# Kernel optimization log

Hardware: AMD Instinct MI355X
Metric: run time of the kernel (lower is better)

Reference implementation:

```python
import jax, jax.numpy as jnp
import numpy as np
import math

B, N, D_IN, D_OUT, H = 8, 1024, 512, 512, 8
DH = D_OUT // H  # 64
SCALE = math.sqrt(DH)

def setup_inputs() -> dict:
    key = jax.random.key(0)
    ks = jax.random.split(key, 10)
    s_in = 1.0 / math.sqrt(D_IN)
    s_out = 1.0 / math.sqrt(D_OUT)
    return {
        "x": jax.random.normal(ks[0], (B, N, D_IN), dtype=jnp.float32),
        "Wq": jax.random.uniform(ks[1], (D_IN, D_OUT), jnp.float32, -s_in, s_in),
        "bq": jnp.zeros((D_OUT,), jnp.float32),
        "Wk": jax.random.uniform(ks[2], (D_IN, D_OUT), jnp.float32, -s_in, s_in),
        "bk": jnp.zeros((D_OUT,), jnp.float32),
        "Wv": jax.random.uniform(ks[3], (D_IN, D_OUT), jnp.float32, -s_in, s_in),
        "bv": jnp.zeros((D_OUT,), jnp.float32),
        "Wo": jax.random.uniform(ks[4], (D_OUT, D_OUT), jnp.float32, -s_out, s_out),
        "bo": jnp.zeros((D_OUT,), jnp.float32),
        # external distance-based positional bias buffer (num_heads, N, N)
        "pos_bias": 0.01 * jax.random.normal(ks[5], (H, N, N), dtype=jnp.float32),
    }

def reference(x, Wq, bq, Wk, bk, Wv, bv, Wo, bo, pos_bias):
    Bx, Nx, _ = x.shape
    # QKV projections -> (B, H, N, DH)
    def split_heads(t):
        return t.reshape(Bx, Nx, H, DH).transpose(0, 2, 1, 3)
    q = split_heads(x @ Wq + bq)
    k = split_heads(x @ Wk + bk)
    v = split_heads(x @ Wv + bv)
    # scaled dot-product scores with additive positional bias
    scores = jnp.einsum('bhnd,bhmd->bhnm', q, k) / SCALE + pos_bias[None]
    attn = jax.nn.softmax(scores, axis=-1)  # dropout p=0 (eval)
    out = jnp.einsum('bhnm,bhmd->bhnd', attn, v)
    out = out.transpose(0, 2, 1, 3).reshape(Bx, Nx, D_OUT)  # concat heads
    return out @ Wo + bo
```

## Files before the change

### kernel.cpp

```cpp
#include <hip/hip_runtime.h>
#include <hip/hip_bf16.h>
#include <stdint.h>


typedef __attribute__((ext_vector_type(4))) float f32x4;
typedef __attribute__((ext_vector_type(8))) short s16x8;
typedef __attribute__((ext_vector_type(4))) unsigned short u16x4;

union FragAB { s16x8 v; u16x4 h[2]; unsigned u[4]; };

#define LOG2E 1.44269504089f
#define QSCALE (0.125f * LOG2E)

__device__ __forceinline__ unsigned short f2b(float f) {
  unsigned u = __builtin_bit_cast(unsigned, f);
  u = (u + 0x7FFFu + ((u >> 16) & 1u)) >> 16;
  return (unsigned short)u;
}
__device__ __forceinline__ unsigned pack2(float lo, float hi) {
  return ((unsigned)f2b(hi) << 16) | (unsigned)f2b(lo);
}

__global__ __launch_bounds__(256) void prep_k(const float* __restrict__ x,
                                              unsigned short* __restrict__ xb,
                                              const float* __restrict__ W0,
                                              const float* __restrict__ W1,
                                              const float* __restrict__ W2,
                                              const float* __restrict__ W3,
                                              unsigned short* __restrict__ Wt) {
  __shared__ float ld[64][68];
  const int t = threadIdx.x;
  if (blockIdx.x < 4096) {
    int idx = blockIdx.x * 256 + t;
    f32x4 v = ((const f32x4*)x)[idx];
    u16x4 o;
#pragma unroll
    for (int j = 0; j < 4; j++) o[j] = f2b(v[j]);
    ((u16x4*)xb)[idx] = o;
    return;
  }
  const int bid2 = blockIdx.x - 4096;
  const int widx = bid2 >> 6;
  const int tile = bid2 & 63;
  const int trow = tile >> 3, tcol = tile & 7;
  const float* W = widx == 0 ? W0 : widx == 1 ? W1 : widx == 2 ? W2 : W3;
  const int r = t >> 2, cc = (t & 3) * 16;
  const float* src = W + (size_t)(trow * 64 + r) * 512 + tcol * 64 + cc;
#pragma unroll
  for (int u = 0; u < 4; u++)
    ((f32x4*)&ld[r][cc])[u] = ((const f32x4*)src)[u];
  __syncthreads();
  unsigned short* dst = Wt + ((size_t)widx << 18) + (size_t)(tcol * 64 + r) * 512 +
                        trow * 64 + cc;
#pragma unroll
  for (int u = 0; u < 4; u++) {
    u16x4 o;
#pragma unroll
    for (int e = 0; e < 4; e++) o[e] = f2b(ld[cc + u * 4 + e][r]);
    ((u16x4*)dst)[u] = o;
  }
}

__global__ __launch_bounds__(256, 2) void gemm_qkv_k(const unsigned short* __restrict__ A,
                                                     const unsigned short* __restrict__ Bt,
                                                     const float* __restrict__ bq,
                                                     const float* __restrict__ bk,
                                                     const float* __restrict__ bv,
                                                     unsigned short* __restrict__ outp) {
  __shared__ unsigned short At[2][128][36];
  __shared__ unsigned short Bts[2][128][36];
  const int tid = threadIdx.x;
  const int lane = tid & 63;
  const int w = tid >> 6;
  const int wm = w >> 1, wn = w & 1;
  const int g = lane >> 4, c = lane & 15;
  const int bn0 = (blockIdx.x % 12) * 128;
  const int bm0 = (blockIdx.x / 12) * 128;
  const int srow = tid >> 1;
  const int scol = (tid & 1) * 16;

  f32x4 acc[4][4];
#pragma unroll
  for (int i = 0; i < 4; i++)
#pragma unroll
    for (int j = 0; j < 4; j++) acc[i][j] = f32x4{0.f, 0.f, 0.f, 0.f};

  u16x4 ra[4], rb[4];
  auto ld = [&](int kt) {
    const u16x4* pa = (const u16x4*)(A + (size_t)(bm0 + srow) * 512 + kt * 32 + scol);
    const u16x4* pb = (const u16x4*)(Bt + (size_t)(bn0 + srow) * 512 + kt * 32 + scol);
#pragma unroll
    for (int j = 0; j < 4; j++) { ra[j] = pa[j]; rb[j] = pb[j]; }
  };
  auto st = [&](int b) {
    u16x4* da = (u16x4*)&At[b][srow][scol];
    u16x4* db = (u16x4*)&Bts[b][srow][scol];
#pragma unroll
    for (int j = 0; j < 4; j++) { da[j] = ra[j]; db[j] = rb[j]; }
  };

  ld(0); st(0);
  __syncthreads();

  for (int kt = 0; kt < 16; ++kt) {
    const int cb = kt & 1;
    if (kt < 15) ld(kt + 1);

    FragAB af[4], bf[4];
#pragma unroll
    for (int mi = 0; mi < 4; mi++) {
      const u16x4* p = (const u16x4*)&At[cb][wm * 64 + mi * 16 + c][g * 8];
      af[mi].h[0] = p[0]; af[mi].h[1] = p[1];
    }
#pragma unroll
    for (int ni = 0; ni < 4; ni++) {
      const u16x4* p = (const u16x4*)&Bts[cb][wn * 64 + ni * 16 + c][g * 8];
      bf[ni].h[0] = p[0]; bf[ni].h[1] = p[1];
    }
    __builtin_amdgcn_s_setprio(1);
#pragma unroll
    for (int mi = 0; mi < 4; mi++)
#pragma unroll
      for (int ni = 0; ni < 4; ni++)
        acc[mi][ni] = __builtin_amdgcn_mfma_f32_16x16x32_bf16(af[mi].v, bf[ni].v,
                                                              acc[mi][ni], 0, 0, 0);
    __builtin_amdgcn_s_setprio(0);

    if (kt < 15) {
      st(cb ^ 1);
      __syncthreads();
    }
  }

  const int qkv = (bn0 + wn * 64) >> 9;
  const float* bp = qkv == 0 ? bq : (qkv == 1 ? bk : bv);
  const float scale = qkv == 0 ? QSCALE : 1.0f;
#pragma unroll
  for (int mi = 0; mi < 4; mi++) {
#pragma unroll
    for (int ni = 0; ni < 4; ni++) {
      const int col = bn0 + wn * 64 + ni * 16 + c;
      const int c9 = col & 511;
      const float bvv = bp[c9];
#pragma unroll
      for (int m = 0; m < 4; m++) {
        const int row = bm0 + wm * 64 + mi * 16 + g * 4 + m;
        const float v = (acc[mi][ni][m] + bvv) * scale;
        const int b = row >> 10, n = row & 1023;
        const int hh = c9 >> 6, d = col & 63;
        outp[((size_t)qkv << 22) + ((size_t)((b << 3) + hh) << 16) +
             ((size_t)n << 6) + d] = f2b(v);
      }
    }
  }
}

__global__ __launch_bounds__(256, 2) void gemm_o_k(const unsigned short* __restrict__ A,
                                                   const unsigned short* __restrict__ Bt,
                                                   const float* __restrict__ bias,
                                                   float* __restrict__ outp) {
  __shared__ unsigned short At[2][128][36];
  __shared__ unsigned short Bts[2][128][36];
  const int tid = threadIdx.x;
  const int lane = tid & 63;
  const int w = tid >> 6;
  const int wm = w >> 1, wn = w & 1;
  const int g = lane >> 4, c = lane & 15;
  const int bn0 = (blockIdx.x & 3) * 128;
  const int bm0 = (blockIdx.x >> 2) * 128;
  const int srow = tid >> 1;
  const int scol = (tid & 1) * 16;

  f32x4 acc[4][4];
#pragma unroll
  for (int i = 0; i < 4; i++)
#pragma unroll
    for (int j = 0; j < 4; j++) acc[i][j] = f32x4{0.f, 0.f, 0.f, 0.f};

  u16x4 ra[4], rb[4];
  auto ld = [&](int kt) {
    const u16x4* pa = (const u16x4*)(A + (size_t)(bm0 + srow) * 512 + kt * 32 + scol);
    const u16x4* pb = (const u16x4*)(Bt + (size_t)(bn0 + srow) * 512 + kt * 32 + scol);
#pragma unroll
    for (int j = 0; j < 4; j++) { ra[j] = pa[j]; rb[j] = pb[j]; }
  };
  auto st = [&](int b) {
    u16x4* da = (u16x4*)&At[b][srow][scol];
    u16x4* db = (u16x4*)&Bts[b][srow][scol];
#pragma unroll
    for (int j = 0; j < 4; j++) { da[j] = ra[j]; db[j] = rb[j]; }
  };

  ld(0); st(0);
  __syncthreads();

  for (int kt = 0; kt < 16; ++kt) {
    const int cb = kt & 1;
    if (kt < 15) ld(kt + 1);

    FragAB af[4], bf[4];
#pragma unroll
    for (int mi = 0; mi < 4; mi++) {
      const u16x4* p = (const u16x4*)&At[cb][wm * 64 + mi * 16 + c][g * 8];
      af[mi].h[0] = p[0]; af[mi].h[1] = p[1];
    }
#pragma unroll
    for (int ni = 0; ni < 4; ni++) {
      const u16x4* p = (const u16x4*)&Bts[cb][wn * 64 + ni * 16 + c][g * 8];
      bf[ni].h[0] = p[0]; bf[ni].h[1] = p[1];
    }
    __builtin_amdgcn_s_setprio(1);
#pragma unroll
    for (int mi = 0; mi < 4; mi++)
#pragma unroll
      for (int ni = 0; ni < 4; ni++)
        acc[mi][ni] = __builtin_amdgcn_mfma_f32_16x16x32_bf16(af[mi].v, bf[ni].v,
                                                              acc[mi][ni], 0, 0, 0);
    __builtin_amdgcn_s_setprio(0);

    if (kt < 15) {
      st(cb ^ 1);
      __syncthreads();
    }
  }

#pragma unroll
  for (int mi = 0; mi < 4; mi++) {
#pragma unroll
    for (int ni = 0; ni < 4; ni++) {
      const int col = bn0 + wn * 64 + ni * 16 + c;
      const float bv = bias[col];
#pragma unroll
      for (int m = 0; m < 4; m++) {
        const int row = bm0 + wm * 64 + mi * 16 + g * 4 + m;
        outp[(size_t)row * 512 + col] = acc[mi][ni][m] + bv;
      }
    }
  }
}

__global__ __launch_bounds__(512, 4) void attn_k(const unsigned short* __restrict__ Qb,
                                                 const unsigned short* __restrict__ Kb,
                                                 const unsigned short* __restrict__ Vb,
                                                 const float* __restrict__ pos_bias,
                                                 unsigned short* __restrict__ ao) {
  __shared__ unsigned short Klds[2][64][68];
  __shared__ unsigned short Vtlds[2][64][68];
  __shared__ unsigned short Plds[8][16][68];

  const int tid = threadIdx.x;
  const int lane = tid & 63;
  const int w = tid >> 6;
  const int g = lane >> 4, c = lane & 15;
  const int L = blockIdx.x;
  const int qt = L >> 6;
  const int bh = (L & 7) + 8 * ((L >> 3) & 7);
  const int h = bh & 7;
  const size_t bhq = (size_t)bh << 16;
  const int q0 = qt * 128 + w * 16;

  FragAB aq[2];
#pragma unroll
  for (int kk = 0; kk < 2; kk++) {
    const u16x4* p =
        (const u16x4*)(Qb + bhq + ((size_t)(q0 + c) << 6) + kk * 32 + g * 8);
    aq[kk].h[0] = p[0]; aq[kk].h[1] = p[1];
  }

  f32x4 acco[4];
#pragma unroll
  for (int nd = 0; nd < 4; nd++) acco[nd] = f32x4{0.f, 0.f, 0.f, 0.f};
  float lsum = 0.f;

  const int krow = tid >> 4;
  const int kslot = (tid & 15) * 4;
  const int vd = tid & 63;
  const int vs = w;

  u16x4 kr[2], vr[2];
  auto stageLoad = [&](int k0n) {
    kr[0] = *(const u16x4*)(Kb + bhq + ((size_t)(k0n + krow) << 6) + kslot);
    kr[1] = *(const u16x4*)(Kb + bhq + ((size_t)(k0n + krow + 32) << 6) + kslot);
    const unsigned short* pv = Vb + bhq + ((size_t)(k0n + vs * 8) << 6) + vd;
    union { unsigned short s[8]; u16x4 v[2]; } vv;
#pragma unroll
    for (int j = 0; j < 8; j++) vv.s[j] = pv[(size_t)j << 6];
    vr[0] = vv.v[0]; vr[1] = vv.v[1];
  };
  auto stageWrite = [&](int b) {
    *(u16x4*)&Klds[b][krow][kslot] = kr[0];
    *(u16x4*)&Klds[b][krow + 32][kslot] = kr[1];
    *(u16x4*)&Vtlds[b][vd][vs * 8] = vr[0];
    *(u16x4*)&Vtlds[b][vd][vs * 8 + 4] = vr[1];
  };

  const float* pbB = pos_bias + ((size_t)h << 20) + ((size_t)(q0 + c) << 10) + 4 * g;

  stageLoad(0);
  stageWrite(0);
  __syncthreads();

  for (int kt = 0; kt < 16; ++kt) {
    const int buf = kt & 1;
    const int k0 = kt << 6;
    if (kt < 15) stageLoad(k0 + 64);

    f32x4 pb[4];
#pragma unroll
    for (int ni = 0; ni < 4; ni++) pb[ni] = *(const f32x4*)(pbB + k0 + 16 * ni);

    FragAB bk[4][2];
#pragma unroll
    for (int ni = 0; ni < 4; ni++)
#pragma unroll
      for (int kk = 0; kk < 2; kk++) {
        const u16x4* p = (const u16x4*)&Klds[buf][ni * 16 + c][kk * 32 + g * 8];
        bk[ni][kk].h[0] = p[0]; bk[ni][kk].h[1] = p[1];
      }
    f32x4 sT[4];
    __builtin_amdgcn_s_setprio(1);
#pragma unroll
    for (int ni = 0; ni < 4; ni++) {
      f32x4 s = f32x4{0.f, 0.f, 0.f, 0.f};
      s = __builtin_amdgcn_mfma_f32_16x16x32_bf16(bk[ni][0].v, aq[0].v, s, 0, 0, 0);
      s = __builtin_amdgcn_mfma_f32_16x16x32_bf16(bk[ni][1].v, aq[1].v, s, 0, 0, 0);
      sT[ni] = s;
    }
    __builtin_amdgcn_s_setprio(0);

#pragma unroll
    for (int ni = 0; ni < 4; ni++) {
      const float p0 = __builtin_amdgcn_exp2f(fmaf(pb[ni][0], LOG2E, sT[ni][0]));
      const float p1 = __builtin_amdgcn_exp2f(fmaf(pb[ni][1], LOG2E, sT[ni][1]));
      const float p2 = __builtin_amdgcn_exp2f(fmaf(pb[ni][2], LOG2E, sT[ni][2]));
      const float p3 = __builtin_amdgcn_exp2f(fmaf(pb[ni][3], LOG2E, sT[ni][3]));
      lsum += (p0 + p1) + (p2 + p3);
      *(unsigned*)&Plds[w][c][16 * ni + 4 * g]     = pack2(p0, p1);
      *(unsigned*)&Plds[w][c][16 * ni + 4 * g + 2] = pack2(p2, p3);
    }

    asm volatile("s_waitcnt lgkmcnt(0)" ::: "memory");

    FragAB paf[2], vb2[4][2];
#pragma unroll
    for (int kc = 0; kc < 2; kc++) {
      const u16x4* p = (const u16x4*)&Plds[w][c][kc * 32 + g * 8];
      paf[kc].h[0] = p[0]; paf[kc].h[1] = p[1];
    }
#pragma unroll
    for (int nd = 0; nd < 4; nd++)
#pragma unroll
      for (int kc = 0; kc < 2; kc++) {
        const u16x4* p = (const u16x4*)&Vtlds[buf][nd * 16 + c][kc * 32 + g * 8];
        vb2[nd][kc].h[0] = p[0]; vb2[nd][kc].h[1] = p[1];
      }
    __builtin_amdgcn_s_setprio(1);
#pragma unroll
    for (int nd = 0; nd < 4; nd++) {
      acco[nd] = __builtin_amdgcn_mfma_f32_16x16x32_bf16(paf[0].v, vb2[nd][0].v,
                                                         acco[nd], 0, 0, 0);
      acco[nd] = __builtin_amdgcn_mfma_f32_16x16x32_bf16(paf[1].v, vb2[nd][1].v,
                                                         acco[nd], 0, 0, 0);
    }
    __builtin_amdgcn_s_setprio(0);

    if (kt < 15) {
      stageWrite(buf ^ 1);
      __syncthreads();
    }
  }

  float l = lsum;
  l += __shfl_xor(l, 16);
  l += __shfl_xor(l, 32);
  const float inv_c = 1.f / l;
  const int b = bh >> 3;
#pragma unroll
  for (int m = 0; m < 4; m++) {
    const float invm = __shfl(inv_c, g * 4 + m);
    const int n = q0 + g * 4 + m;
#pragma unroll
    for (int nd = 0; nd < 4; nd++) {
      ao[((size_t)(b * 1024 + n) << 9) + h * 64 + nd * 16 + c] =
          f2b(acco[nd][m] * invm);
    }
  }
}

extern "C" void kernel_launch(void* const* d_in, const int* in_sizes, int n_in,
                              void* d_out, int out_size, void* d_ws, size_t ws_size,
                              hipStream_t stream) {
  (void)in_sizes; (void)n_in; (void)out_size; (void)ws_size;
  const float* x  = (const float*)d_in[0];
  const float* Wq = (const float*)d_in[1];
  const float* bq = (const float*)d_in[2];
  const float* Wk = (const float*)d_in[3];
  const float* bk = (const float*)d_in[4];
  const float* Wv = (const float*)d_in[5];
  const float* bv = (const float*)d_in[6];
  const float* Wo = (const float*)d_in[7];
  const float* bo = (const float*)d_in[8];
  const float* pbias = (const float*)d_in[9];

  char* p = (char*)d_ws;
  unsigned short* xb  = (unsigned short*)p; p += (size_t)8192 * 512 * 2;
  unsigned short* WT  = (unsigned short*)p; p += (size_t)4 * 512 * 512 * 2;
  unsigned short* Qb  = (unsigned short*)p; p += (size_t)3 * 64 * 1024 * 64 * 2;
  unsigned short* AO  = (unsigned short*)p;

  unsigned short* WoT = WT + (size_t)3 * 512 * 512;
  unsigned short* Kb  = Qb + (size_t)64 * 1024 * 64;
  unsigned short* Vb  = Kb + (size_t)64 * 1024 * 64;

  prep_k<<<4352, 256, 0, stream>>>(x, xb, Wq, Wk, Wv, Wo, WT);
  gemm_qkv_k<<<768, 256, 0, stream>>>(xb, WT, bq, bk, bv, Qb);
  attn_k<<<512, 512, 0, stream>>>(Qb, Kb, Vb, pbias, AO);
  gemm_o_k<<<256, 256, 0, stream>>>(AO, WoT, bo, (float*)d_out);
}
```

Measured before the change: 89.30 us.

## Process two query row tiles per wave in attention to reuse K/V fragments

The attention kernel now uses 256-thread blocks where each of 4 waves handles 32 query rows (two 16-row MFMA tiles) instead of 8 waves with 16 rows each. K and V fragments read from LDS are reused across both row tiles, which halves LDS fragment reads per unit of work. K/V staging loads are widened to 8-element vectors and P tiles are stored as uint2. The trade-off is higher register pressure from doubled accumulators and score tiles, and fewer waves per block to hide latency.

```diff
diff --git a/kernel.cpp b/kernel.cpp
--- a/kernel.cpp
+++ b/kernel.cpp
@@ -6,6 +6,7 @@
 typedef __attribute__((ext_vector_type(4))) float f32x4;
 typedef __attribute__((ext_vector_type(8))) short s16x8;
 typedef __attribute__((ext_vector_type(4))) unsigned short u16x4;
+typedef __attribute__((ext_vector_type(8))) unsigned short u16x8;
 
 union FragAB { s16x8 v; u16x4 h[2]; unsigned u[4]; };
 
@@ -239,14 +240,14 @@
   }
 }
 
-__global__ __launch_bounds__(512, 4) void attn_k(const unsigned short* __restrict__ Qb,
+__global__ __launch_bounds__(256, 2) void attn_k(const unsigned short* __restrict__ Qb,
                                                  const unsigned short* __restrict__ Kb,
                                                  const unsigned short* __restrict__ Vb,
                                                  const float* __restrict__ pos_bias,
                                                  unsigned short* __restrict__ ao) {
   __shared__ unsigned short Klds[2][64][68];
   __shared__ unsigned short Vtlds[2][64][68];
-  __shared__ unsigned short Plds[8][16][68];
+  __shared__ unsigned short Plds[4][32][68];
 
   const int tid = threadIdx.x;
   const int lane = tid & 63;
@@ -257,41 +258,44 @@
   const int bh = (L & 7) + 8 * ((L >> 3) & 7);
   const int h = bh & 7;
   const size_t bhq = (size_t)bh << 16;
-  const int q0 = qt * 128 + w * 16;
-
-  FragAB aq[2];
-#pragma unroll
-  for (int kk = 0; kk < 2; kk++) {
-    const u16x4* p =
-        (const u16x4*)(Qb + bhq + ((size_t)(q0 + c) << 6) + kk * 32 + g * 8);
-    aq[kk].h[0] = p[0]; aq[kk].h[1] = p[1];
-  }
-
-  f32x4 acco[4];
-#pragma unroll
-  for (int nd = 0; nd < 4; nd++) acco[nd] = f32x4{0.f, 0.f, 0.f, 0.f};
-  float lsum = 0.f;
-
-  const int krow = tid >> 4;
-  const int kslot = (tid & 15) * 4;
+  const int q0 = qt * 128 + w * 32;
+
+  FragAB aq[2][2];
+#pragma unroll
+  for (int mi = 0; mi < 2; mi++)
+#pragma unroll
+    for (int kk = 0; kk < 2; kk++) {
+      const u16x4* p = (const u16x4*)(Qb + bhq + ((size_t)(q0 + mi * 16 + c) << 6) +
+                                      kk * 32 + g * 8);
+      aq[mi][kk].h[0] = p[0]; aq[mi][kk].h[1] = p[1];
+    }
+
+  f32x4 acco[2][4];
+#pragma unroll
+  for (int mi = 0; mi < 2; mi++)
+#pragma unroll
+    for (int nd = 0; nd < 4; nd++) acco[mi][nd] = f32x4{0.f, 0.f, 0.f, 0.f};
+  float lsum[2] = {0.f, 0.f};
+
+  const int krow = tid >> 3;
+  const int kcol = (tid & 7) * 8;
   const int vd = tid & 63;
-  const int vs = w;
-
-  u16x4 kr[2], vr[2];
+  const int vs = tid >> 6;
+
+  u16x8 kr0, kr1;
+  union { unsigned short s[16]; u16x8 v[2]; } vv;
   auto stageLoad = [&](int k0n) {
-    kr[0] = *(const u16x4*)(Kb + bhq + ((size_t)(k0n + krow) << 6) + kslot);
-    kr[1] = *(const u16x4*)(Kb + bhq + ((size_t)(k0n + krow + 32) << 6) + kslot);
-    const unsigned short* pv = Vb + bhq + ((size_t)(k0n + vs * 8) << 6) + vd;
-    union { unsigned short s[8]; u16x4 v[2]; } vv;
-#pragma unroll
-    for (int j = 0; j < 8; j++) vv.s[j] = pv[(size_t)j << 6];
-    vr[0] = vv.v[0]; vr[1] = vv.v[1];
+    kr0 = *(const u16x8*)(Kb + bhq + ((size_t)(k0n + krow) << 6) + kcol);
+    kr1 = *(const u16x8*)(Kb + bhq + ((size_t)(k0n + krow + 32) << 6) + kcol);
+    const unsigned short* pv = Vb + bhq + ((size_t)(k0n + vs * 16) << 6) + vd;
+#pragma unroll
+    for (int j = 0; j < 16; j++) vv.s[j] = pv[(size_t)j << 6];
   };
   auto stageWrite = [&](int b) {
-    *(u16x4*)&Klds[b][krow][kslot] = kr[0];
-    *(u16x4*)&Klds[b][krow + 32][kslot] = kr[1];
-    *(u16x4*)&Vtlds[b][vd][vs * 8] = vr[0];
-    *(u16x4*)&Vtlds[b][vd][vs * 8 + 4] = vr[1];
+    *(u16x8*)&Klds[b][krow][kcol] = kr0;
+    *(u16x8*)&Klds[b][krow + 32][kcol] = kr1;
+    *(u16x8*)&Vtlds[b][vd][vs * 16] = vv.v[0];
+    *(u16x8*)&Vtlds[b][vd][vs * 16 + 8] = vv.v[1];
   };
 
   const float* pbB = pos_bias + ((size_t)h << 20) + ((size_t)(q0 + c) << 10) + 4 * g;
@@ -305,9 +309,12 @@
     const int k0 = kt << 6;
     if (kt < 15) stageLoad(k0 + 64);
 
-    f32x4 pb[4];
-#pragma unroll
-    for (int ni = 0; ni < 4; ni++) pb[ni] = *(const f32x4*)(pbB + k0 + 16 * ni);
+    f32x4 pb[2][4];
+#pragma unroll
+    for (int mi = 0; mi < 2; mi++)
+#pragma unroll
+      for (int ni = 0; ni < 4; ni++)
+        pb[mi][ni] = *(const f32x4*)(pbB + (mi << 14) + k0 + 16 * ni);
 
     FragAB bk[4][2];
 #pragma unroll
@@ -317,36 +324,44 @@
         const u16x4* p = (const u16x4*)&Klds[buf][ni * 16 + c][kk * 32 + g * 8];
         bk[ni][kk].h[0] = p[0]; bk[ni][kk].h[1] = p[1];
       }
-    f32x4 sT[4];
+    f32x4 sT[2][4];
     __builtin_amdgcn_s_setprio(1);
 #pragma unroll
-    for (int ni = 0; ni < 4; ni++) {
-      f32x4 s = f32x4{0.f, 0.f, 0.f, 0.f};
-      s = __builtin_amdgcn_mfma_f32_16x16x32_bf16(bk[ni][0].v, aq[0].v, s, 0, 0, 0);
-      s = __builtin_amdgcn_mfma_f32_16x16x32_bf16(bk[ni][1].v, aq[1].v, s, 0, 0, 0);
-      sT[ni] = s;
-    }
+    for (int mi = 0; mi < 2; mi++)
+#pragma unroll
+      for (int ni = 0; ni < 4; ni++) {
+        f32x4 s = f32x4{0.f, 0.f, 0.f, 0.f};
+        s = __builtin_amdgcn_mfma_f32_16x16x32_bf16(bk[ni][0].v, aq[mi][0].v, s, 0, 0, 0);
+        s = __builtin_amdgcn_mfma_f32_16x16x32_bf16(bk[ni][1].v, aq[mi][1].v, s, 0, 0, 0);
+        sT[mi][ni] = s;
+      }
     __builtin_amdgcn_s_setprio(0);
 
 #pragma unroll
-    for (int ni = 0; ni < 4; ni++) {
-      const float p0 = __builtin_amdgcn_exp2f(fmaf(pb[ni][0], LOG2E, sT[ni][0]));
-      const float p1 = __builtin_amdgcn_exp2f(fmaf(pb[ni][1], LOG2E, sT[ni][1]));
-      const float p2 = __builtin_amdgcn_exp2f(fmaf(pb[ni][2], LOG2E, sT[ni][2]));
-      const float p3 = __builtin_amdgcn_exp2f(fmaf(pb[ni][3], LOG2E, sT[ni][3]));
-      lsum += (p0 + p1) + (p2 + p3);
-      *(unsigned*)&Plds[w][c][16 * ni + 4 * g]     = pack2(p0, p1);
-      *(unsigned*)&Plds[w][c][16 * ni + 4 * g + 2] = pack2(p2, p3);
-    }
+    for (int mi = 0; mi < 2; mi++)
+#pragma unroll
+      for (int ni = 0; ni < 4; ni++) {
+        const float p0 = __builtin_amdgcn_exp2f(fmaf(pb[mi][ni][0], LOG2E, sT[mi][ni][0]));
+        const float p1 = __builtin_amdgcn_exp2f(fmaf(pb[mi][ni][1], LOG2E, sT[mi][ni][1]));
+        const float p2 = __builtin_amdgcn_exp2f(fmaf(pb[mi][ni][2], LOG2E, sT[mi][ni][2]));
+        const float p3 = __builtin_amdgcn_exp2f(fmaf(pb[mi][ni][3], LOG2E, sT[mi][ni][3]));
+        lsum[mi] += (p0 + p1) + (p2 + p3);
+        uint2 two;
+        two.x = pack2(p0, p1);
+        two.y = pack2(p2, p3);
+        *(uint2*)&Plds[w][mi * 16 + c][16 * ni + 4 * g] = two;
+      }
 
     asm volatile("s_waitcnt lgkmcnt(0)" ::: "memory");
 
-    FragAB paf[2], vb2[4][2];
-#pragma unroll
-    for (int kc = 0; kc < 2; kc++) {
-      const u16x4* p = (const u16x4*)&Plds[w][c][kc * 32 + g * 8];
-      paf[kc].h[0] = p[0]; paf[kc].h[1] = p[1];
-    }
+    FragAB paf[2][2], vb2[4][2];
+#pragma unroll
+    for (int mi = 0; mi < 2; mi++)
+#pragma unroll
+      for (int kc = 0; kc < 2; kc++) {
+        const u16x4* p = (const u16x4*)&Plds[w][mi * 16 + c][kc * 32 + g * 8];
+        paf[mi][kc].h[0] = p[0]; paf[mi][kc].h[1] = p[1];
+      }
 #pragma unroll
     for (int nd = 0; nd < 4; nd++)
 #pragma unroll
@@ -356,12 +371,14 @@
       }
     __builtin_amdgcn_s_setprio(1);
 #pragma unroll
-    for (int nd = 0; nd < 4; nd++) {
-      acco[nd] = __builtin_amdgcn_mfma_f32_16x16x32_bf16(paf[0].v, vb2[nd][0].v,
-                                                         acco[nd], 0, 0, 0);
-      acco[nd] = __builtin_amdgcn_mfma_f32_16x16x32_bf16(paf[1].v, vb2[nd][1].v,
-                                                         acco[nd], 0, 0, 0);
-    }
+    for (int mi = 0; mi < 2; mi++)
+#pragma unroll
+      for (int nd = 0; nd < 4; nd++) {
+        acco[mi][nd] = __builtin_amdgcn_mfma_f32_16x16x32_bf16(paf[mi][0].v, vb2[nd][0].v,
+                                                               acco[mi][nd], 0, 0, 0);
+        acco[mi][nd] = __builtin_amdgcn_mfma_f32_16x16x32_bf16(paf[mi][1].v, vb2[nd][1].v,
+                                                               acco[mi][nd], 0, 0, 0);
+      }
     __builtin_amdgcn_s_setprio(0);
 
     if (kt < 15) {
@@ -370,19 +387,22 @@
     }
   }
 
-  float l = lsum;
-  l += __shfl_xor(l, 16);
-  l += __shfl_xor(l, 32);
-  const float inv_c = 1.f / l;
   const int b = bh >> 3;
 #pragma unroll
-  for (int m = 0; m < 4; m++) {
-    const float invm = __shfl(inv_c, g * 4 + m);
-    const int n = q0 + g * 4 + m;
-#pragma unroll
-    for (int nd = 0; nd < 4; nd++) {
-      ao[((size_t)(b * 1024 + n) << 9) + h * 64 + nd * 16 + c] =
-          f2b(acco[nd][m] * invm);
+  for (int mi = 0; mi < 2; mi++) {
+    float l = lsum[mi];
+    l += __shfl_xor(l, 16);
+    l += __shfl_xor(l, 32);
+    const float inv_c = 1.f / l;
+#pragma unroll
+    for (int m = 0; m < 4; m++) {
+      const float invm = __shfl(inv_c, g * 4 + m);
+      const int n = q0 + mi * 16 + g * 4 + m;
+#pragma unroll
+      for (int nd = 0; nd < 4; nd++) {
+        ao[((size_t)(b * 1024 + n) << 9) + h * 64 + nd * 16 + c] =
+            f2b(acco[mi][nd][m] * invm);
+      }
     }
   }
 }
@@ -414,6 +434,6 @@
 
   prep_k<<<4352, 256, 0, stream>>>(x, xb, Wq, Wk, Wv, Wo, WT);
   gemm_qkv_k<<<768, 256, 0, stream>>>(xb, WT, bq, bk, bv, Qb);
-  attn_k<<<512, 512, 0, stream>>>(Qb, Kb, Vb, pbias, AO);
+  attn_k<<<512, 256, 0, stream>>>(Qb, Kb, Vb, pbias, AO);
   gemm_o_k<<<256, 256, 0, stream>>>(AO, WoT, bo, (float*)d_out);
 }
```

Measured after the change: 88.09 us. About the same (-1.4%).
